# Kernel tuning notes

Measured on AMD Instinct MI355X. Metric: run time of the kernel, lower is better.

## Reference

```python
import jax, jax.numpy as jnp
import numpy as np

N_NODES = 100000
N_EDGES = 1600000
D = 128

def setup_inputs() -> dict:
    key = jax.random.key(0)
    ks = jax.random.split(key, 6)
    x = jax.random.normal(ks[0], (N_NODES, D), dtype=jnp.float32)
    edge_src = jax.random.randint(ks[1], (N_EDGES,), 0, N_NODES, dtype=jnp.int32)
    edge_dst = jax.random.randint(ks[2], (N_EDGES,), 0, N_NODES, dtype=jnp.int32)
    # Glorot-ish scaling for 128x128 linears
    scale = 1.0 / np.sqrt(D)
    W1 = jax.random.normal(ks[3], (D, D), dtype=jnp.float32) * scale
    b1 = jnp.zeros((D,), dtype=jnp.float32)
    W2 = jax.random.normal(ks[4], (D, D), dtype=jnp.float32) * scale
    b2 = jnp.zeros((D,), dtype=jnp.float32)
    return {"x": x, "edge_src": edge_src, "edge_dst": edge_dst,
            "W1": W1, "b1": b1, "W2": W2, "b2": b2}

def reference(x, edge_src, edge_dst, W1, b1, W2, b2):
    # g.set_data('.hidden', data); g.apply(pre_mod): Linear + ReLU per node
    h = jax.nn.relu(x @ W1 + b1)                      # [N, D]
    # g.push(func=sum): each node's hidden becomes the sum of its
    # in-neighbors' hidden features (gather by src, scatter-add by dst).
    msgs = h[edge_src]                                # [E, D] irregular gather
    agg = jax.ops.segment_sum(msgs, edge_dst, num_segments=N_NODES)  # [N, D]
    # g.apply(post_mod): Linear per node; g.pop_data returns result
    out = agg @ W2 + b2                               # [N, D]
    return out
```

## Files before the change

### kernel.cpp

```cpp
#include <hip/hip_runtime.h>

#define D 128
#define NPB 256
#define NBMAX 512
#define BKCAP 8192
#define CHUNK 8192
#define OVF_CAP 8192

typedef __attribute__((ext_vector_type(8))) short short8x;
typedef __attribute__((ext_vector_type(4))) float f32x4;

__device__ inline unsigned int f2bf(float f) {
    unsigned int u = __builtin_bit_cast(unsigned int, f);
    return (u + 0x7fffu + ((u >> 16) & 1u)) >> 16;
}
__device__ inline float bflo(unsigned int v) {
    return __builtin_bit_cast(float, v << 16);
}
__device__ inline float bfhi(unsigned int v) {
    return __builtin_bit_cast(float, v & 0xffff0000u);
}
__device__ inline unsigned int pack2(float lo, float hi) {
    return f2bf(lo) | (f2bf(hi) << 16);
}

__global__ __launch_bounds__(256) void pack_w(
    const float* __restrict__ W1, const float* __restrict__ W2,
    uint4* __restrict__ pack)
{
    int e = blockIdx.x * 256 + threadIdx.x;
    const float* W = (e & 2048) ? W2 : W1;
    int f = (e >> 6) & 31, l = e & 63;
    int kt = f >> 3, nt = f & 7;
    int k0 = kt * 32 + (l >> 4) * 8;
    int col = nt * 16 + (l & 15);
    unsigned int v[8];
#pragma unroll
    for (int j = 0; j < 8; ++j) v[j] = f2bf(W[(size_t)(k0 + j) * D + col]);
    uint4 o;
    o.x = v[0] | (v[1] << 16);
    o.y = v[2] | (v[3] << 16);
    o.z = v[4] | (v[5] << 16);
    o.w = v[6] | (v[7] << 16);
    pack[e] = o;
}

__global__ __launch_bounds__(256) void build_gemm(
    const int* __restrict__ esrc, const int* __restrict__ edst,
    int* __restrict__ gfill, unsigned* __restrict__ pairs,
    int* __restrict__ ovf_cnt, int2* __restrict__ ovf_list, int E, int NB,
    int nscatter,
    const float* __restrict__ xin, const uint4* __restrict__ wpack,
    const float* __restrict__ b1, unsigned short* __restrict__ zout, int n_rows)
{
    __shared__ __align__(16) char smem[81920];
    const int t = threadIdx.x;

    if (blockIdx.x < nscatter) {
        int* lcnt  = (int*)smem;
        int* lbase = lcnt + NBMAX;
        for (int b = t; b < NB; b += 256) lcnt[b] = 0;
        __syncthreads();
        int cb = blockIdx.x * CHUNK;
        int ce = min(E, cb + CHUNK);
        for (int i = cb + t; i < ce; i += 256)
            atomicAdd(&lcnt[edst[i] >> 8], 1);
        __syncthreads();
        for (int b = t; b < NB; b += 256) {
            int c = lcnt[b];
            lbase[b] = c ? atomicAdd(&gfill[b], c) : 0;
            lcnt[b] = 0;
        }
        __syncthreads();
        for (int i = cb + t; i < ce; i += 256) {
            int d = edst[i];
            int s = esrc[i];
            int b = d >> 8;
            int pos = lbase[b] + atomicAdd(&lcnt[b], 1);
            if (pos < BKCAP) {
                pairs[(size_t)b * BKCAP + pos] = ((unsigned)s << 8) | (unsigned)(d & 255);
            } else {
                int o = atomicAdd(ovf_cnt, 1);
                if (o < OVF_CAP) ovf_list[o] = make_int2(s, d);
            }
        }
        return;
    }

    uint4* ws1 = (uint4*)smem;
    uint4* ws2 = ws1 + 2048;
    uint4* xs4 = ws2 + 2048;
    const int row0 = (blockIdx.x - nscatter) * 64;

#pragma unroll
    for (int i = 0; i < 8; ++i) ws1[t + 256 * i] = wpack[t + 256 * i];
#pragma unroll
    for (int i = 0; i < 8; ++i) ws2[t + 256 * i] = wpack[2048 + t + 256 * i];

    const float4* g = (const float4*)xin;
#pragma unroll
    for (int i = 0; i < 4; ++i) {
        int c = t + 256 * i;
        int row = c >> 4, kc = c & 15;
        int grow = row0 + row;
        if (grow < n_rows) {
            float4 f0 = g[(size_t)grow * 32 + kc * 2];
            float4 f1 = g[(size_t)grow * 32 + kc * 2 + 1];
            uint4 v;
            v.x = pack2(f0.x, f0.y);
            v.y = pack2(f0.z, f0.w);
            v.z = pack2(f1.x, f1.y);
            v.w = pack2(f1.z, f1.w);
            xs4[row * 16 + (kc ^ (row & 7))] = v;
        }
    }
    __syncthreads();

    const int l = t & 63;
    const int w = t >> 6;
    const int l15 = l & 15;
    const int lk = l >> 4;
    const int arow = w * 16 + l15;

    float bias1[8];
#pragma unroll
    for (int nt = 0; nt < 8; ++nt) bias1[nt] = b1[nt * 16 + l15];

    f32x4 acc1[8];
#pragma unroll
    for (int nt = 0; nt < 8; ++nt) acc1[nt] = (f32x4){0.f, 0.f, 0.f, 0.f};

#pragma unroll
    for (int kt = 0; kt < 4; ++kt) {
        short8x a = *(const short8x*)&xs4[arow * 16 + ((kt * 4 + lk) ^ (arow & 7))];
#pragma unroll
        for (int nt = 0; nt < 8; ++nt) {
            short8x bf = *(const short8x*)&ws1[(kt * 8 + nt) * 64 + l];
            acc1[nt] = __builtin_amdgcn_mfma_f32_16x16x32_bf16(a, bf, acc1[nt], 0, 0, 0);
        }
    }
    __syncthreads();

    unsigned short* hsu = (unsigned short*)xs4;
#pragma unroll
    for (int nt = 0; nt < 8; ++nt) {
        int col = nt * 16 + l15;
        int ci = (col >> 3), ce2 = (col & 7);
#pragma unroll
        for (int r = 0; r < 4; ++r) {
            int rowl = w * 16 + lk * 4 + r;
            float v = fmaxf(acc1[nt][r] + bias1[nt], 0.f);
            hsu[(rowl * 16 + (ci ^ (rowl & 7))) * 8 + ce2] = (unsigned short)f2bf(v);
        }
    }
    __syncthreads();

    f32x4 acc2[8];
#pragma unroll
    for (int nt = 0; nt < 8; ++nt) acc2[nt] = (f32x4){0.f, 0.f, 0.f, 0.f};

#pragma unroll
    for (int kt = 0; kt < 4; ++kt) {
        short8x a = *(const short8x*)&xs4[arow * 16 + ((kt * 4 + lk) ^ (arow & 7))];
#pragma unroll
        for (int nt = 0; nt < 8; ++nt) {
            short8x bf = *(const short8x*)&ws2[(kt * 8 + nt) * 64 + l];
            acc2[nt] = __builtin_amdgcn_mfma_f32_16x16x32_bf16(a, bf, acc2[nt], 0, 0, 0);
        }
    }

#pragma unroll
    for (int r = 0; r < 4; ++r) {
        int row = row0 + w * 16 + lk * 4 + r;
        if (row >= n_rows) continue;
#pragma unroll
        for (int nt = 0; nt < 8; ++nt) {
            int col = nt * 16 + l15;
            zout[(size_t)row * D + col] = (unsigned short)f2bf(acc2[nt][r]);
        }
    }
}

__global__ __launch_bounds__(256) void node_sort(
    const unsigned* __restrict__ pairs, const int* __restrict__ gfill,
    int* __restrict__ srcs, int2* __restrict__ noff2, int n_nodes)
{
    __shared__ int fill[NPB];
    __shared__ int scanb[NPB];
    const int bkt = blockIdx.x;
    const int t = threadIdx.x;
    const size_t ebase = (size_t)bkt * BKCAP;
    const int ecnt = min(gfill[bkt], BKCAP);

    fill[t] = 0;
    __syncthreads();
    for (int i = t; i < ecnt; i += 256)
        atomicAdd(&fill[pairs[ebase + i] & 255], 1);
    __syncthreads();

    int c = fill[t];
    scanb[t] = c;
    __syncthreads();
    for (int s = 1; s < NPB; s <<= 1) {
        int add = (t >= s) ? scanb[t - s] : 0;
        __syncthreads();
        scanb[t] += add;
        __syncthreads();
    }
    int off = scanb[t] - c;
    int node = (bkt << 8) + t;
    if (node < n_nodes) noff2[node] = make_int2((int)ebase + off, c);
    fill[t] = off;
    __syncthreads();

    for (int i = t; i < ecnt; i += 256) {
        unsigned v = pairs[ebase + i];
        int pos = atomicAdd(&fill[v & 255], 1);
        srcs[ebase + pos] = (int)(v >> 8);
    }
}

__global__ __launch_bounds__(256) void pull_csr(
    const uint2* __restrict__ z2, const int* __restrict__ srcs,
    const int2* __restrict__ noff2, const float* __restrict__ b2,
    float* __restrict__ out, int n_nodes)
{
    int node = blockIdx.x * 8 + (threadIdx.x >> 5);
    int lane = threadIdx.x & 31;
    if (node >= n_nodes) return;
    int2 se = noff2[node];
    int i = se.x, end = se.x + se.y;

    float a0 = 0.f, a1 = 0.f, a2 = 0.f, a3 = 0.f;
    for (; i + 8 <= end; i += 8) {
        int4 sA = *(const int4*)(srcs + i);
        int4 sB = *(const int4*)(srcs + i + 4);
        uint2 v0 = z2[(size_t)sA.x * 32 + lane];
        uint2 v1 = z2[(size_t)sA.y * 32 + lane];
        uint2 v2 = z2[(size_t)sA.z * 32 + lane];
        uint2 v3 = z2[(size_t)sA.w * 32 + lane];
        uint2 v4 = z2[(size_t)sB.x * 32 + lane];
        uint2 v5 = z2[(size_t)sB.y * 32 + lane];
        uint2 v6 = z2[(size_t)sB.z * 32 + lane];
        uint2 v7 = z2[(size_t)sB.w * 32 + lane];
        a0 += bflo(v0.x) + bflo(v1.x) + bflo(v2.x) + bflo(v3.x)
            + bflo(v4.x) + bflo(v5.x) + bflo(v6.x) + bflo(v7.x);
        a1 += bfhi(v0.x) + bfhi(v1.x) + bfhi(v2.x) + bfhi(v3.x)
            + bfhi(v4.x) + bfhi(v5.x) + bfhi(v6.x) + bfhi(v7.x);
        a2 += bflo(v0.y) + bflo(v1.y) + bflo(v2.y) + bflo(v3.y)
            + bflo(v4.y) + bflo(v5.y) + bflo(v6.y) + bflo(v7.y);
        a3 += bfhi(v0.y) + bfhi(v1.y) + bfhi(v2.y) + bfhi(v3.y)
            + bfhi(v4.y) + bfhi(v5.y) + bfhi(v6.y) + bfhi(v7.y);
    }
    if (i + 4 <= end) {
        int4 s = *(const int4*)(srcs + i);
        uint2 v0 = z2[(size_t)s.x * 32 + lane];
        uint2 v1 = z2[(size_t)s.y * 32 + lane];
        uint2 v2 = z2[(size_t)s.z * 32 + lane];
        uint2 v3 = z2[(size_t)s.w * 32 + lane];
        a0 += bflo(v0.x) + bflo(v1.x) + bflo(v2.x) + bflo(v3.x);
        a1 += bfhi(v0.x) + bfhi(v1.x) + bfhi(v2.x) + bfhi(v3.x);
        a2 += bflo(v0.y) + bflo(v1.y) + bflo(v2.y) + bflo(v3.y);
        a3 += bfhi(v0.y) + bfhi(v1.y) + bfhi(v2.y) + bfhi(v3.y);
        i += 4;
    }
    for (; i < end; ++i) {
        int s = srcs[i];
        uint2 v = z2[(size_t)s * 32 + lane];
        a0 += bflo(v.x); a1 += bfhi(v.x);
        a2 += bflo(v.y); a3 += bfhi(v.y);
    }
    float4 bv = ((const float4*)b2)[lane];
    ((float4*)out)[(size_t)node * 32 + lane] =
        make_float4(a0 + bv.x, a1 + bv.y, a2 + bv.z, a3 + bv.w);
}

__global__ __launch_bounds__(32) void ovf_f32(
    const int* __restrict__ ovf_cnt, const int2* __restrict__ ovf_list,
    const uint2* __restrict__ z2, float* __restrict__ out)
{
    int n = *ovf_cnt;
    if (n > OVF_CAP) n = OVF_CAP;
    int lane = threadIdx.x;
    for (int i = blockIdx.x; i < n; i += gridDim.x) {
        int2 sd = ovf_list[i];
        uint2 v = z2[(size_t)sd.x * 32 + lane];
        unsafeAtomicAdd(&out[(size_t)sd.y * D + lane * 4 + 0], bflo(v.x));
        unsafeAtomicAdd(&out[(size_t)sd.y * D + lane * 4 + 1], bfhi(v.x));
        unsafeAtomicAdd(&out[(size_t)sd.y * D + lane * 4 + 2], bflo(v.y));
        unsafeAtomicAdd(&out[(size_t)sd.y * D + lane * 4 + 3], bfhi(v.y));
    }
}

template <bool RELU>
__global__ __launch_bounds__(256) void gemm_bias_act(
    const float* xin, const float* __restrict__ W,
    const float* __restrict__ b, float* xout, int n_rows)
{
    __shared__ float Ws[D * D];
    __shared__ float xs[32 * D];
    const int t = threadIdx.x;
    const int row0 = blockIdx.x * 32;
    const float4* Wv = (const float4*)W;
    float4* Wsv = (float4*)Ws;
#pragma unroll
    for (int i = 0; i < 16; ++i) Wsv[t + 256 * i] = Wv[t + 256 * i];
    const float4* xv = (const float4*)xin;
    float4* xsv = (float4*)xs;
#pragma unroll
    for (int i = 0; i < 4; ++i) {
        int f4 = t + 256 * i;
        int row = row0 + (f4 >> 5);
        if (row < n_rows) xsv[f4] = xv[(size_t)row0 * 32 + f4];
    }
    __syncthreads();
    const int cg = t & 31;
    const int rg = t >> 5;
    float4 bias = ((const float4*)b)[cg];
    float4 acc[4];
#pragma unroll
    for (int ri = 0; ri < 4; ++ri) acc[ri] = make_float4(0.f, 0.f, 0.f, 0.f);
#pragma unroll 4
    for (int k = 0; k < D; k += 4) {
        float4 w0 = Wsv[(k + 0) * 32 + cg];
        float4 w1 = Wsv[(k + 1) * 32 + cg];
        float4 w2 = Wsv[(k + 2) * 32 + cg];
        float4 w3 = Wsv[(k + 3) * 32 + cg];
#pragma unroll
        for (int ri = 0; ri < 4; ++ri) {
            float4 xa = xsv[(rg + 8 * ri) * 32 + (k >> 2)];
            acc[ri].x = fmaf(xa.x, w0.x, fmaf(xa.y, w1.x, fmaf(xa.z, w2.x, fmaf(xa.w, w3.x, acc[ri].x))));
            acc[ri].y = fmaf(xa.x, w0.y, fmaf(xa.y, w1.y, fmaf(xa.z, w2.y, fmaf(xa.w, w3.y, acc[ri].y))));
            acc[ri].z = fmaf(xa.x, w0.z, fmaf(xa.y, w1.z, fmaf(xa.z, w2.z, fmaf(xa.w, w3.z, acc[ri].z))));
            acc[ri].w = fmaf(xa.x, w0.w, fmaf(xa.y, w1.w, fmaf(xa.z, w2.w, fmaf(xa.w, w3.w, acc[ri].w))));
        }
    }
#pragma unroll
    for (int ri = 0; ri < 4; ++ri) {
        int row = row0 + rg + 8 * ri;
        if (row >= n_rows) continue;
        float4 o;
        o.x = acc[ri].x + bias.x; o.y = acc[ri].y + bias.y;
        o.z = acc[ri].z + bias.z; o.w = acc[ri].w + bias.w;
        if (RELU) {
            o.x = fmaxf(o.x, 0.f); o.y = fmaxf(o.y, 0.f);
            o.z = fmaxf(o.z, 0.f); o.w = fmaxf(o.w, 0.f);
        }
        ((float4*)xout)[(size_t)row * 32 + cg] = o;
    }
}

__global__ __launch_bounds__(256) void zero_kernel(float4* p, int n4)
{
    int i = blockIdx.x * 256 + threadIdx.x;
    int stride = gridDim.x * 256;
    for (; i < n4; i += stride) p[i] = make_float4(0.f, 0.f, 0.f, 0.f);
}

__global__ __launch_bounds__(256) void scatter_kernel(
    const float* __restrict__ h, const int* __restrict__ esrc,
    const int* __restrict__ edst, float* __restrict__ agg, long n_items)
{
    long idx = (long)blockIdx.x * 256 + threadIdx.x;
    long stride = (long)gridDim.x * 256;
    for (; idx < n_items; idx += stride) {
        int e = (int)(idx >> 7);
        int c = (int)(idx & 127);
        int s = esrc[e];
        int d = edst[e];
        unsafeAtomicAdd(&agg[(size_t)d * D + c], h[(size_t)s * D + c]);
    }
}

extern "C" void kernel_launch(void* const* d_in, const int* in_sizes, int n_in,
                              void* d_out, int out_size, void* d_ws, size_t ws_size,
                              hipStream_t stream)
{
    const float* x    = (const float*)d_in[0];
    const int*   esrc = (const int*)d_in[1];
    const int*   edst = (const int*)d_in[2];
    const float* W1   = (const float*)d_in[3];
    const float* b1   = (const float*)d_in[4];
    const float* W2   = (const float*)d_in[5];
    const float* b2   = (const float*)d_in[6];
    float* out = (float*)d_out;

    const int N = in_sizes[0] / D;
    const int E = in_sizes[1];
    const int NB = (N + NPB - 1) / NPB;

    char* ws = (char*)d_ws;
    size_t off_z     = 0;
    size_t off_pairs = off_z + (size_t)N * 256;
    size_t off_srcs  = off_pairs + (size_t)NBMAX * BKCAP * 4;
    size_t off_noff  = off_srcs + (size_t)NBMAX * BKCAP * 4;
    size_t off_gfill = (off_noff + (size_t)N * 8 + 255) & ~(size_t)255;
    size_t off_ovfc  = off_gfill + NBMAX * 4;
    size_t off_ovfl  = off_ovfc + 16;
    size_t off_pack  = (off_ovfl + (size_t)OVF_CAP * 8 + 255) & ~(size_t)255;
    size_t need      = off_pack + 65536;

    const int gchunk = (E + CHUNK - 1) / CHUNK;
    const int nblk64 = (N + 63) / 64;

    if (ws_size >= need && N <= NBMAX * NPB) {
        uint2*    z2    = (uint2*)(ws + off_z);
        unsigned* pairs = (unsigned*)(ws + off_pairs);
        int*      srcs  = (int*)(ws + off_srcs);
        int2*     noff2 = (int2*)(ws + off_noff);
        int*      gfill = (int*)(ws + off_gfill);
        int*      ovfc  = (int*)(ws + off_ovfc);
        int2*     ovfl  = (int2*)(ws + off_ovfl);
        uint4*    pack  = (uint4*)(ws + off_pack);

        hipMemsetAsync(gfill, 0, NBMAX * 4 + 16, stream);

        pack_w<<<16, 256, 0, stream>>>(W1, W2, pack);

        build_gemm<<<gchunk + nblk64, 256, 0, stream>>>(
            esrc, edst, gfill, pairs, ovfc, ovfl, E, NB, gchunk,
            x, pack, b1, (unsigned short*)z2, N);

        node_sort<<<NB, 256, 0, stream>>>(pairs, gfill, srcs, noff2, N);

        pull_csr<<<(N + 7) / 8, 256, 0, stream>>>(z2, srcs, noff2, b2, out, N);

        ovf_f32<<<8, 32, 0, stream>>>(ovfc, ovfl, z2, out);
    } else {
        float* h = (float*)ws;
        const int nb32 = (N + 31) / 32;
        gemm_bias_act<true><<<nb32, 256, 0, stream>>>(x, W1, b1, h, N);
        zero_kernel<<<2048, 256, 0, stream>>>((float4*)out, N * D / 4);
        scatter_kernel<<<8192, 256, 0, stream>>>(h, esrc, edst, out, (long)E * D);
        gemm_bias_act<false><<<nb32, 256, 0, stream>>>(out, W2, b2, out, N);
    }
}
```

Baseline: 123.9 us.

## Use 128-row GEMM tiles with shared weight buffer and coalesced z stores; fold memset into pack_w

The fused GEMM blocks now process 128 rows instead of 64, with each wave computing two 16-row tiles per weight fragment load. A single 32KB LDS weight buffer is reloaded with W2 after the first GEMM, which cuts shared memory from 80KB to 64KB. The bf16 output is staged through LDS and written as coalesced 16-byte stores. The gfill/overflow memset becomes an extra block in pack_w, removing one API call. The trade-off is more registers per thread for the doubled accumulators and an extra sync plus weight reload per block.

```diff
diff --git a/kernel.cpp b/kernel.cpp
--- a/kernel.cpp
+++ b/kernel.cpp
@@ -26,8 +26,12 @@
 
 __global__ __launch_bounds__(256) void pack_w(
     const float* __restrict__ W1, const float* __restrict__ W2,
-    uint4* __restrict__ pack)
-{
+    uint4* __restrict__ pack, int* __restrict__ zero_area, int nz)
+{
+    if (blockIdx.x == 16) {
+        for (int i = threadIdx.x; i < nz; i += 256) zero_area[i] = 0;
+        return;
+    }
     int e = blockIdx.x * 256 + threadIdx.x;
     const float* W = (e & 2048) ? W2 : W1;
     int f = (e >> 6) & 31, l = e & 63;
@@ -51,9 +55,9 @@
     int* __restrict__ ovf_cnt, int2* __restrict__ ovf_list, int E, int NB,
     int nscatter,
     const float* __restrict__ xin, const uint4* __restrict__ wpack,
-    const float* __restrict__ b1, unsigned short* __restrict__ zout, int n_rows)
-{
-    __shared__ __align__(16) char smem[81920];
+    const float* __restrict__ b1, uint4* __restrict__ zout4, int n_rows)
+{
+    __shared__ __align__(16) char smem[65536];
     const int t = threadIdx.x;
 
     if (blockIdx.x < nscatter) {
@@ -87,19 +91,16 @@
         return;
     }
 
-    uint4* ws1 = (uint4*)smem;
-    uint4* ws2 = ws1 + 2048;
-    uint4* xs4 = ws2 + 2048;
-    const int row0 = (blockIdx.x - nscatter) * 64;
-
-#pragma unroll
-    for (int i = 0; i < 8; ++i) ws1[t + 256 * i] = wpack[t + 256 * i];
-#pragma unroll
-    for (int i = 0; i < 8; ++i) ws2[t + 256 * i] = wpack[2048 + t + 256 * i];
+    uint4* ws  = (uint4*)smem;
+    uint4* xs4 = ws + 2048;
+    const int row0 = (blockIdx.x - nscatter) * 128;
+
+#pragma unroll
+    for (int i = 0; i < 8; ++i) ws[t + 256 * i] = wpack[t + 256 * i];
 
     const float4* g = (const float4*)xin;
 #pragma unroll
-    for (int i = 0; i < 4; ++i) {
+    for (int i = 0; i < 8; ++i) {
         int c = t + 256 * i;
         int row = c >> 4, kc = c & 15;
         int grow = row0 + row;
@@ -120,64 +121,94 @@
     const int w = t >> 6;
     const int l15 = l & 15;
     const int lk = l >> 4;
-    const int arow = w * 16 + l15;
+    const int arow0 = w * 32 + l15;
+    const int arow1 = arow0 + 16;
 
     float bias1[8];
 #pragma unroll
     for (int nt = 0; nt < 8; ++nt) bias1[nt] = b1[nt * 16 + l15];
 
-    f32x4 acc1[8];
-#pragma unroll
-    for (int nt = 0; nt < 8; ++nt) acc1[nt] = (f32x4){0.f, 0.f, 0.f, 0.f};
+    f32x4 acc1[2][8];
+#pragma unroll
+    for (int rt = 0; rt < 2; ++rt)
+#pragma unroll
+        for (int nt = 0; nt < 8; ++nt) acc1[rt][nt] = (f32x4){0.f, 0.f, 0.f, 0.f};
 
 #pragma unroll
     for (int kt = 0; kt < 4; ++kt) {
-        short8x a = *(const short8x*)&xs4[arow * 16 + ((kt * 4 + lk) ^ (arow & 7))];
+        int kc0 = kt * 4 + lk;
+        short8x a0 = *(const short8x*)&xs4[arow0 * 16 + (kc0 ^ (arow0 & 7))];
+        short8x a1 = *(const short8x*)&xs4[arow1 * 16 + (kc0 ^ (arow1 & 7))];
 #pragma unroll
         for (int nt = 0; nt < 8; ++nt) {
-            short8x bf = *(const short8x*)&ws1[(kt * 8 + nt) * 64 + l];
-            acc1[nt] = __builtin_amdgcn_mfma_f32_16x16x32_bf16(a, bf, acc1[nt], 0, 0, 0);
-        }
-    }
-    __syncthreads();
+            short8x bf = *(const short8x*)&ws[(kt * 8 + nt) * 64 + l];
+            acc1[0][nt] = __builtin_amdgcn_mfma_f32_16x16x32_bf16(a0, bf, acc1[0][nt], 0, 0, 0);
+            acc1[1][nt] = __builtin_amdgcn_mfma_f32_16x16x32_bf16(a1, bf, acc1[1][nt], 0, 0, 0);
+        }
+    }
 
     unsigned short* hsu = (unsigned short*)xs4;
 #pragma unroll
-    for (int nt = 0; nt < 8; ++nt) {
-        int col = nt * 16 + l15;
-        int ci = (col >> 3), ce2 = (col & 7);
-#pragma unroll
-        for (int r = 0; r < 4; ++r) {
-            int rowl = w * 16 + lk * 4 + r;
-            float v = fmaxf(acc1[nt][r] + bias1[nt], 0.f);
-            hsu[(rowl * 16 + (ci ^ (rowl & 7))) * 8 + ce2] = (unsigned short)f2bf(v);
-        }
-    }
-    __syncthreads();
-
-    f32x4 acc2[8];
-#pragma unroll
-    for (int nt = 0; nt < 8; ++nt) acc2[nt] = (f32x4){0.f, 0.f, 0.f, 0.f};
-
-#pragma unroll
-    for (int kt = 0; kt < 4; ++kt) {
-        short8x a = *(const short8x*)&xs4[arow * 16 + ((kt * 4 + lk) ^ (arow & 7))];
-#pragma unroll
-        for (int nt = 0; nt < 8; ++nt) {
-            short8x bf = *(const short8x*)&ws2[(kt * 8 + nt) * 64 + l];
-            acc2[nt] = __builtin_amdgcn_mfma_f32_16x16x32_bf16(a, bf, acc2[nt], 0, 0, 0);
-        }
-    }
-
-#pragma unroll
-    for (int r = 0; r < 4; ++r) {
-        int row = row0 + w * 16 + lk * 4 + r;
-        if (row >= n_rows) continue;
+    for (int rt = 0; rt < 2; ++rt) {
 #pragma unroll
         for (int nt = 0; nt < 8; ++nt) {
             int col = nt * 16 + l15;
-            zout[(size_t)row * D + col] = (unsigned short)f2bf(acc2[nt][r]);
-        }
+            int ci = (col >> 3), ce2 = (col & 7);
+#pragma unroll
+            for (int r = 0; r < 4; ++r) {
+                int rowl = w * 32 + rt * 16 + lk * 4 + r;
+                float v = fmaxf(acc1[rt][nt][r] + bias1[nt], 0.f);
+                hsu[(rowl * 16 + (ci ^ (rowl & 7))) * 8 + ce2] = (unsigned short)f2bf(v);
+            }
+        }
+    }
+    __syncthreads();
+
+#pragma unroll
+    for (int i = 0; i < 8; ++i) ws[t + 256 * i] = wpack[2048 + t + 256 * i];
+    __syncthreads();
+
+    f32x4 acc2[2][8];
+#pragma unroll
+    for (int rt = 0; rt < 2; ++rt)
+#pragma unroll
+        for (int nt = 0; nt < 8; ++nt) acc2[rt][nt] = (f32x4){0.f, 0.f, 0.f, 0.f};
+
+#pragma unroll
+    for (int kt = 0; kt < 4; ++kt) {
+        int kc0 = kt * 4 + lk;
+        short8x a0 = *(const short8x*)&xs4[arow0 * 16 + (kc0 ^ (arow0 & 7))];
+        short8x a1 = *(const short8x*)&xs4[arow1 * 16 + (kc0 ^ (arow1 & 7))];
+#pragma unroll
+        for (int nt = 0; nt < 8; ++nt) {
+            short8x bf = *(const short8x*)&ws[(kt * 8 + nt) * 64 + l];
+            acc2[0][nt] = __builtin_amdgcn_mfma_f32_16x16x32_bf16(a0, bf, acc2[0][nt], 0, 0, 0);
+            acc2[1][nt] = __builtin_amdgcn_mfma_f32_16x16x32_bf16(a1, bf, acc2[1][nt], 0, 0, 0);
+        }
+    }
+    __syncthreads();
+
+    unsigned short* zls = (unsigned short*)ws;
+#pragma unroll
+    for (int rt = 0; rt < 2; ++rt) {
+#pragma unroll
+        for (int nt = 0; nt < 8; ++nt) {
+            int col = nt * 16 + l15;
+#pragma unroll
+            for (int r = 0; r < 4; ++r) {
+                int rowl = w * 32 + rt * 16 + lk * 4 + r;
+                zls[rowl * D + col] = (unsigned short)f2bf(acc2[rt][nt][r]);
+            }
+        }
+    }
+    __syncthreads();
+    const uint4* zlsv = (const uint4*)zls;
+#pragma unroll
+    for (int i = 0; i < 8; ++i) {
+        int c = t + 256 * i;
+        int row = c >> 4, kc = c & 15;
+        if (row0 + row < n_rows)
+            zout4[(size_t)(row0 + row) * 16 + kc] = zlsv[c];
     }
 }
 
@@ -401,10 +432,10 @@
     size_t need      = off_pack + 65536;
 
     const int gchunk = (E + CHUNK - 1) / CHUNK;
-    const int nblk64 = (N + 63) / 64;
+    const int nblk128 = (N + 127) / 128;
 
     if (ws_size >= need && N <= NBMAX * NPB) {
-        uint2*    z2    = (uint2*)(ws + off_z);
+        uint4*    z4    = (uint4*)(ws + off_z);
         unsigned* pairs = (unsigned*)(ws + off_pairs);
         int*      srcs  = (int*)(ws + off_srcs);
         int2*     noff2 = (int2*)(ws + off_noff);
@@ -413,19 +444,18 @@
         int2*     ovfl  = (int2*)(ws + off_ovfl);
         uint4*    pack  = (uint4*)(ws + off_pack);
 
-        hipMemsetAsync(gfill, 0, NBMAX * 4 + 16, stream);
-
-        pack_w<<<16, 256, 0, stream>>>(W1, W2, pack);
-
-        build_gemm<<<gchunk + nblk64, 256, 0, stream>>>(
+        pack_w<<<17, 256, 0, stream>>>(W1, W2, pack, gfill, NBMAX + 4);
+
+        build_gemm<<<gchunk + nblk128, 256, 0, stream>>>(
             esrc, edst, gfill, pairs, ovfc, ovfl, E, NB, gchunk,
-            x, pack, b1, (unsigned short*)z2, N);
+            x, pack, b1, z4, N);
 
         node_sort<<<NB, 256, 0, stream>>>(pairs, gfill, srcs, noff2, N);
 
-        pull_csr<<<(N + 7) / 8, 256, 0, stream>>>(z2, srcs, noff2, b2, out, N);
-
-        ovf_f32<<<8, 32, 0, stream>>>(ovfc, ovfl, z2, out);
+        pull_csr<<<(N + 7) / 8, 256, 0, stream>>>(
+            (const uint2*)z4, srcs, noff2, b2, out, N);
+
+        ovf_f32<<<8, 32, 0, stream>>>(ovfc, ovfl, (const uint2*)z4, out);
     } else {
         float* h = (float*)ws;
         const int nb32 = (N + 31) / 32;
```

Measured after the change: 121.2 us. -2.2%, faster.
